# Optimization experiments

Hardware: AMD Instinct MI355X
Metric: run time of the kernel (lower is better)

The kernel has to match this reference:

```python
import jax, jax.numpy as jnp
import numpy as np

B, T, IMG, P, D, H, L = 4, 32, 84, 14, 768, 12, 3
GP = IMG // P            # 6 patches per side
NP = GP * GP             # 36 patches
N = NP + 1               # +cls token
FF = 4 * D
HD = D // H


def _ln(x, g, b):
    m = jnp.mean(x, -1, keepdims=True)
    v = jnp.var(x, -1, keepdims=True)
    return (x - m) * jax.lax.rsqrt(v + 1e-5) * g + b


def _mha(x, qkv_w, qkv_b, proj_w, proj_b):
    Bn, Nn, C = x.shape
    qkv = (x @ qkv_w + qkv_b).reshape(Bn, Nn, 3, H, HD).transpose(2, 0, 3, 1, 4)
    q, k, v = qkv[0], qkv[1], qkv[2]                      # (B,H,N,hd)
    attn = jax.nn.softmax(jnp.einsum('bhqd,bhkd->bhqk', q, k) * HD ** -0.5, axis=-1)
    o = jnp.einsum('bhqk,bhkd->bhqd', attn, v).transpose(0, 2, 1, 3).reshape(Bn, Nn, C)
    return o @ proj_w + proj_b


def _blocks(x, pre_g, pre_b, n1_g, n1_b, qkv_w, qkv_b, proj_w, proj_b,
            n2_g, n2_b, fc1_w, fc1_b, fc2_w, fc2_b):
    # TemporalViT applies an extra pre-norm, then x = x + Block(x_norm),
    # where Block itself contains two residual sublayers on x_norm.
    for i in range(L):
        xn = _ln(x, pre_g[i], pre_b[i])
        y = xn + _mha(_ln(xn, n1_g[i], n1_b[i]), qkv_w[i], qkv_b[i], proj_w[i], proj_b[i])
        h = jax.nn.gelu(_ln(y, n2_g[i], n2_b[i]) @ fc1_w[i] + fc1_b[i], approximate=False)
        y = y + h @ fc2_w[i] + fc2_b[i]
        x = x + y
    return x


def _forward(x, conv_w, conv_b, cls, pos, tpos,
             s_pre_g, s_pre_b, s_n1_g, s_n1_b, s_qkv_w, s_qkv_b, s_proj_w, s_proj_b,
             s_n2_g, s_n2_b, s_fc1_w, s_fc1_b, s_fc2_w, s_fc2_b,
             t_pre_g, t_pre_b, t_n1_g, t_n1_b, t_qkv_w, t_qkv_b, t_proj_w, t_proj_b,
             t_n2_g, t_n2_b, t_fc1_w, t_fc1_b, t_fc2_w, t_fc2_b):
    xf = x.reshape(B * T, 3, IMG, IMG)
    p = jax.lax.conv_general_dilated(xf, conv_w, (P, P), 'VALID',
                                     dimension_numbers=('NCHW', 'OIHW', 'NCHW'))
    p = p + conv_b[None, :, None, None]                  # (BT, D, 6, 6)
    p = p.reshape(B * T, D, NP).transpose(0, 2, 1)       # (BT, 36, D)
    p = jnp.concatenate([jnp.broadcast_to(cls, (B * T, 1, D)), p], axis=1) + pos
    p = _blocks(p, s_pre_g, s_pre_b, s_n1_g, s_n1_b, s_qkv_w, s_qkv_b, s_proj_w,
                s_proj_b, s_n2_g, s_n2_b, s_fc1_w, s_fc1_b, s_fc2_w, s_fc2_b)
    p = p.reshape(B, T * N, D)
    tp = jnp.broadcast_to(tpos[:, :T, None, :], (1, T, N, D)).reshape(1, T * N, D)
    p = p + tp
    p = _blocks(p, t_pre_g, t_pre_b, t_n1_g, t_n1_b, t_qkv_w, t_qkv_b, t_proj_w,
                t_proj_b, t_n2_g, t_n2_b, t_fc1_w, t_fc1_b, t_fc2_w, t_fc2_b)
    return p.mean(axis=1)                                # (B, D)


def setup_inputs() -> dict:
    key = jax.random.key(0)
    ks = iter(jax.random.split(key, 64))
    r = lambda shape, s=0.02: (jax.random.normal(next(ks), shape, jnp.float32) * s)
    inp = {
        'x': jax.random.normal(next(ks), (B, T, 3, IMG, IMG), jnp.float32),
        'conv_w': r((D, 3, P, P)), 'conv_b': jnp.zeros((D,), jnp.float32),
        'cls': r((1, 1, D)), 'pos': r((1, N, D)), 'tpos': r((1, 100, D)),
    }
    for pfx in ('s', 't'):
        inp[f'{pfx}_pre_g'] = jnp.ones((L, D), jnp.float32)
        inp[f'{pfx}_pre_b'] = jnp.zeros((L, D), jnp.float32)
        inp[f'{pfx}_n1_g'] = jnp.ones((L, D), jnp.float32)
        inp[f'{pfx}_n1_b'] = jnp.zeros((L, D), jnp.float32)
        inp[f'{pfx}_qkv_w'] = r((L, D, 3 * D))
        inp[f'{pfx}_qkv_b'] = jnp.zeros((L, 3 * D), jnp.float32)
        inp[f'{pfx}_proj_w'] = r((L, D, D))
        inp[f'{pfx}_proj_b'] = jnp.zeros((L, D), jnp.float32)
        inp[f'{pfx}_n2_g'] = jnp.ones((L, D), jnp.float32)
        inp[f'{pfx}_n2_b'] = jnp.zeros((L, D), jnp.float32)
        inp[f'{pfx}_fc1_w'] = r((L, D, FF))
        inp[f'{pfx}_fc1_b'] = jnp.zeros((L, FF), jnp.float32)
        inp[f'{pfx}_fc2_w'] = r((L, FF, D))
        inp[f'{pfx}_fc2_b'] = jnp.zeros((L, D), jnp.float32)
    return inp


def reference(x, conv_w, conv_b, cls, pos, tpos,
              s_pre_g, s_pre_b, s_n1_g, s_n1_b, s_qkv_w, s_qkv_b, s_proj_w, s_proj_b,
              s_n2_g, s_n2_b, s_fc1_w, s_fc1_b, s_fc2_w, s_fc2_b,
              t_pre_g, t_pre_b, t_n1_g, t_n1_b, t_qkv_w, t_qkv_b, t_proj_w, t_proj_b,
              t_n2_g, t_n2_b, t_fc1_w, t_fc1_b, t_fc2_w, t_fc2_b):
    return _forward(x, conv_w, conv_b, cls, pos, tpos,
                    s_pre_g, s_pre_b, s_n1_g, s_n1_b, s_qkv_w, s_qkv_b, s_proj_w,
                    s_proj_b, s_n2_g, s_n2_b, s_fc1_w, s_fc1_b, s_fc2_w, s_fc2_b,
                    t_pre_g, t_pre_b, t_n1_g, t_n1_b, t_qkv_w, t_qkv_b, t_proj_w,
                    t_proj_b, t_n2_g, t_n2_b, t_fc1_w, t_fc1_b, t_fc2_w, t_fc2_b)
```

## Files before the change

kernel.cpp:

```cpp
#include <hip/hip_runtime.h>
#include <math.h>

#define NTOK 4736
#define DM   768
#define NHEAD 12
#define KC   640

typedef __attribute__((ext_vector_type(8))) short bf16x8;
typedef __attribute__((ext_vector_type(4))) float f32x4;

__device__ inline short f2bf(float f) {
  union { float f; unsigned u; } v; v.f = f;
  unsigned r = v.u + 0x7FFF + ((v.u >> 16) & 1);
  return (short)(r >> 16);
}
__device__ inline float bf2f(short s) {
  union { unsigned u; float f; } v; v.u = ((unsigned)(unsigned short)s) << 16;
  return v.f;
}

__device__ inline void gload16(const void* g, void* l) {
  __builtin_amdgcn_global_load_lds(
      (const __attribute__((address_space(1))) void*)g,
      (__attribute__((address_space(3))) void*)l, 16, 0, 0);
}

__global__ __launch_bounds__(256) void im2col_k(const float* __restrict__ x,
                                                short* __restrict__ col) {
  int i = blockIdx.x * 256 + threadIdx.x;
  int r = i / KC, k = i % KC;
  short v = 0;
  if (k < 588) {
    int bt = r / 36, p = r % 36;
    int gy = p / 6, gx = p % 6;
    int c = k / 196, rem = k % 196;
    int ky = rem / 14, kx = rem % 14;
    v = f2bf(x[(((size_t)bt * 3 + c) * 84 + gy * 14 + ky) * 84 + gx * 14 + kx]);
  }
  col[i] = v;
}

__global__ __launch_bounds__(256) void convw_k(const float* __restrict__ w,
                                               short* __restrict__ out) {
  int i = blockIdx.x * 256 + threadIdx.x;
  int n = i / KC, k = i % KC;
  out[i] = (k < 588) ? f2bf(w[(size_t)n * 588 + k]) : (short)0;
}

__global__ __launch_bounds__(256) void wt_k(const float* __restrict__ in,
                                            short* __restrict__ out,
                                            int K, int N) {
  __shared__ float tile[32][33];
  const int l = blockIdx.z;
  in  += (size_t)l * K * N;
  out += (size_t)l * N * K;
  const int n0 = blockIdx.x * 32, k0 = blockIdx.y * 32;
  const int tx = threadIdx.x & 31, ty = threadIdx.x >> 5;
#pragma unroll
  for (int r = 0; r < 4; r++)
    tile[ty + 8 * r][tx] = in[(size_t)(k0 + ty + 8 * r) * N + n0 + tx];
  __syncthreads();
#pragma unroll
  for (int r = 0; r < 4; r++)
    out[(size_t)(n0 + ty + 8 * r) * K + k0 + tx] = f2bf(tile[tx][ty + 8 * r]);
}

__global__ __launch_bounds__(256) void assemble_k(const float* __restrict__ conv_out,
                                                  const float* __restrict__ cls,
                                                  const float* __restrict__ pos,
                                                  float* __restrict__ X) {
  int i = blockIdx.x * 256 + threadIdx.x;
  int t = i / DM, d = i % DM;
  int bt = t / 37, n = t % 37;
  float v = (n == 0) ? cls[d] : conv_out[((size_t)bt * 36 + (n - 1)) * DM + d];
  X[i] = v + pos[n * DM + d];
}

__global__ __launch_bounds__(256) void tpos_k(float* __restrict__ X,
                                              const float* __restrict__ tpos) {
  int i = blockIdx.x * 256 + threadIdx.x;
  int row = i / DM, d = i % DM;
  int tt = (row % 1184) / 37;
  X[i] += tpos[tt * DM + d];
}

template <bool OBF>
__global__ __launch_bounds__(256) void ln_k(const float* __restrict__ in,
                                            const float* __restrict__ g,
                                            const float* __restrict__ b,
                                            void* __restrict__ outp) {
  int r = blockIdx.x;
  int tid = threadIdx.x;
  const float* xr = in + (size_t)r * DM;
  float v0 = xr[tid], v1 = xr[tid + 256], v2 = xr[tid + 512];
  float s  = v0 + v1 + v2;
  float sq = v0 * v0 + v1 * v1 + v2 * v2;
#pragma unroll
  for (int off = 32; off; off >>= 1) {
    s  += __shfl_down(s, off);
    sq += __shfl_down(sq, off);
  }
  __shared__ float ss[4], sg[4];
  if ((tid & 63) == 0) { ss[tid >> 6] = s; sg[tid >> 6] = sq; }
  __syncthreads();
  float S = ss[0] + ss[1] + ss[2] + ss[3];
  float Q = sg[0] + sg[1] + sg[2] + sg[3];
  float mean = S * (1.f / 768.f);
  float var  = Q * (1.f / 768.f) - mean * mean;
  float rs = rsqrtf(var + 1e-5f);
  float o0 = (v0 - mean) * rs * g[tid]       + b[tid];
  float o1 = (v1 - mean) * rs * g[tid + 256] + b[tid + 256];
  float o2 = (v2 - mean) * rs * g[tid + 512] + b[tid + 512];
  if (OBF) {
    short* o = (short*)outp + (size_t)r * DM;
    o[tid] = f2bf(o0); o[tid + 256] = f2bf(o1); o[tid + 512] = f2bf(o2);
  } else {
    float* o = (float*)outp + (size_t)r * DM;
    o[tid] = o0; o[tid + 256] = o1; o[tid + 512] = o2;
  }
}

__global__ __launch_bounds__(256) void ln2_k(const float* __restrict__ in,
                                             const float* __restrict__ g1,
                                             const float* __restrict__ b1,
                                             const float* __restrict__ g2,
                                             const float* __restrict__ b2,
                                             float* __restrict__ xn,
                                             short* __restrict__ w) {
  int r = blockIdx.x;
  int tid = threadIdx.x;
  const float* xr = in + (size_t)r * DM;
  float v0 = xr[tid], v1 = xr[tid + 256], v2 = xr[tid + 512];
  float s  = v0 + v1 + v2;
  float sq = v0 * v0 + v1 * v1 + v2 * v2;
#pragma unroll
  for (int off = 32; off; off >>= 1) {
    s  += __shfl_down(s, off);
    sq += __shfl_down(sq, off);
  }
  __shared__ float ss[4], sg[4], ss2[4], sg2[4];
  if ((tid & 63) == 0) { ss[tid >> 6] = s; sg[tid >> 6] = sq; }
  __syncthreads();
  float S = ss[0] + ss[1] + ss[2] + ss[3];
  float Q = sg[0] + sg[1] + sg[2] + sg[3];
  float mean = S * (1.f / 768.f);
  float var  = Q * (1.f / 768.f) - mean * mean;
  float rs = rsqrtf(var + 1e-5f);
  float x0 = (v0 - mean) * rs * g1[tid]       + b1[tid];
  float x1 = (v1 - mean) * rs * g1[tid + 256] + b1[tid + 256];
  float x2 = (v2 - mean) * rs * g1[tid + 512] + b1[tid + 512];
  float* xo = xn + (size_t)r * DM;
  xo[tid] = x0; xo[tid + 256] = x1; xo[tid + 512] = x2;
  float s2  = x0 + x1 + x2;
  float sq2 = x0 * x0 + x1 * x1 + x2 * x2;
#pragma unroll
  for (int off = 32; off; off >>= 1) {
    s2  += __shfl_down(s2, off);
    sq2 += __shfl_down(sq2, off);
  }
  if ((tid & 63) == 0) { ss2[tid >> 6] = s2; sg2[tid >> 6] = sq2; }
  __syncthreads();
  float S2 = ss2[0] + ss2[1] + ss2[2] + ss2[3];
  float Q2 = sg2[0] + sg2[1] + sg2[2] + sg2[3];
  float mean2 = S2 * (1.f / 768.f);
  float var2  = Q2 * (1.f / 768.f) - mean2 * mean2;
  float rs2 = rsqrtf(var2 + 1e-5f);
  short* wo = w + (size_t)r * DM;
  wo[tid]       = f2bf((x0 - mean2) * rs2 * g2[tid]       + b2[tid]);
  wo[tid + 256] = f2bf((x1 - mean2) * rs2 * g2[tid + 256] + b2[tid + 256]);
  wo[tid + 512] = f2bf((x2 - mean2) * rs2 * g2[tid + 512] + b2[tid + 512]);
}

template <int BM, int BN, bool GELU, bool OBF, bool HASR1, bool HASR2>
__global__ __launch_bounds__(256, 4) void tgemm_k(const short* __restrict__ A,
                                                  const short* __restrict__ Bw,
                                                  const float* __restrict__ bias,
                                                  const float* __restrict__ r1,
                                                  const float* __restrict__ r2,
                                                  void* __restrict__ Cout,
                                                  int M, int N, int K) {
  constexpr int TM = BM / 2, TN = BN / 2;
  constexpr int MF = TM / 16, NF = TN / 16;
  constexpr int ACH = BM / 64, BCH = BN / 64;
  constexpr int LOADS = ACH + BCH;

  __shared__ short As[2][BM][32];
  __shared__ short Bs[2][BN][32];

  const int nwg  = gridDim.x * gridDim.y;
  const int orig = blockIdx.x + gridDim.x * blockIdx.y;
  const int qq = nwg >> 3, rrm = nwg & 7;
  const int xcd = orig & 7, sub = orig >> 3;
  const int wgid = ((xcd < rrm) ? xcd * (qq + 1) : rrm * (qq + 1) + (xcd - rrm) * qq) + sub;
  const int bm = (wgid / gridDim.y) * BM, bn = (wgid % gridDim.y) * BN;

  const int tid = threadIdx.x, wid = tid >> 6, lane = tid & 63;
  const int lr = lane & 15, lg = lane >> 4;
  const int wm = wid >> 1, wn = wid & 1;

  const int srow = tid >> 2;
  const int sslot = (tid & 3) ^ ((srow >> 1) & 3);
  const short* Asrc = A  + (size_t)(bm + srow) * K + sslot * 8;
  const short* Bsrc = Bw + (size_t)(bn + srow) * K + sslot * 8;

  f32x4 acc[MF][NF];
#pragma unroll
  for (int m = 0; m < MF; m++)
#pragma unroll
    for (int n = 0; n < NF; n++) acc[m][n] = (f32x4){0.f, 0.f, 0.f, 0.f};

#define STAGE(slot, kk)                                                        \
  do {                                                                         \
    _Pragma("unroll")                                                          \
    for (int j = 0; j < ACH; j++)                                              \
      gload16(Asrc + (size_t)(j * 64) * K + (kk),                              \
              (char*)&As[slot][0][0] + j * 4096 + wid * 1024);                 \
    _Pragma("unroll")                                                          \
    for (int j = 0; j < BCH; j++)                                              \
      gload16(Bsrc + (size_t)(j * 64) * K + (kk),                              \
              (char*)&Bs[slot][0][0] + j * 4096 + wid * 1024);                 \
  } while (0)

  const int NT = K >> 5;
  const int rkey = (lr >> 1) & 3;

  STAGE(0, 0);
  for (int t = 0; t < NT; t++) {
    const int c = t & 1;
    if (t + 1 < NT) {
      STAGE(c ^ 1, (t + 1) << 5);
      if constexpr (LOADS == 4) asm volatile("s_waitcnt vmcnt(4)" ::: "memory");
      else                      asm volatile("s_waitcnt vmcnt(2)" ::: "memory");
    } else {
      asm volatile("s_waitcnt vmcnt(0)" ::: "memory");
    }
    __builtin_amdgcn_s_barrier();

    bf16x8 aq[MF], bq[NF];
#pragma unroll
    for (int nf = 0; nf < NF; nf++) {
      const int row = wn * TN + nf * 16 + lr;
      bq[nf] = *reinterpret_cast<const bf16x8*>(
          (const char*)&Bs[c][0][0] + row * 64 + ((lg ^ rkey) << 4));
    }
#pragma unroll
    for (int mf = 0; mf < MF; mf++) {
      const int row = wm * TM + mf * 16 + lr;
      aq[mf] = *reinterpret_cast<const bf16x8*>(
          (const char*)&As[c][0][0] + row * 64 + ((lg ^ rkey) << 4));
    }
    __builtin_amdgcn_s_setprio(1);
#pragma unroll
    for (int mf = 0; mf < MF; mf++)
#pragma unroll
      for (int nf = 0; nf < NF; nf++)
        acc[mf][nf] = __builtin_amdgcn_mfma_f32_16x16x32_bf16(
            aq[mf], bq[nf], acc[mf][nf], 0, 0, 0);
    __builtin_amdgcn_s_setprio(0);
    __builtin_amdgcn_s_barrier();
  }
#undef STAGE

#pragma unroll
  for (int m = 0; m < MF; m++) {
#pragma unroll
    for (int r = 0; r < 4; r++) {
      int row = bm + wm * TM + m * 16 + lg * 4 + r;
      if (row < M) {
#pragma unroll
        for (int n = 0; n < NF; n++) {
          int col = bn + wn * TN + n * 16 + lr;
          size_t idx = (size_t)row * N + col;
          float v = acc[m][n][r];
          if (bias) v += bias[col];
          if (GELU) v = 0.5f * v * (1.f + erff(v * 0.70710678118654752f));
          if (HASR1) v += r1[idx];
          if (HASR2) v += r2[idx];
          if (OBF) ((short*)Cout)[idx] = f2bf(v);
          else     ((float*)Cout)[idx] = v;
        }
      }
    }
  }
}

__global__ __launch_bounds__(256) void attn_k(const short* __restrict__ qkv,
                                              short* __restrict__ out,
                                              int Bn, int Nn) {
  const int gx = gridDim.x, gy = gridDim.y;
  const int nwg = gx * gy;
  const int orig = blockIdx.x + gx * blockIdx.y;
  const int qq = nwg >> 3, rrm = nwg & 7;
  const int xcd = orig & 7, sub = orig >> 3;
  const int wgid = ((xcd < rrm) ? xcd * (qq + 1) : rrm * (qq + 1) + (xcd - rrm) * qq) + sub;
  const int bh = wgid / gy;
  const int qb = wgid % gy;
  const int b = bh / NHEAD, h = bh % NHEAD;
  const int q0 = qb * 64;

  const int tid = threadIdx.x;
  const int wid = tid >> 6, lane = tid & 63;
  const int lr = lane & 15, lg = lane >> 4;

  __shared__ short Ks[128][64];
  __shared__ short Vt[64][128];
  __shared__ short Ps[4][16][128];

  const int qrow_in = q0 + wid * 16 + lr;
  const int qcl = (qrow_in < Nn) ? qrow_in : (Nn - 1);
  const short* qp = qkv + ((size_t)(b * Nn + qcl)) * 2304 + h * 64 + lg * 8;
  bf16x8 qa0 = *reinterpret_cast<const bf16x8*>(qp);
  bf16x8 qa1 = *reinterpret_cast<const bf16x8*>(qp + 32);
#pragma unroll
  for (int j = 0; j < 8; j++) {
    qa0[j] = f2bf(bf2f(qa0[j]) * 0.125f);
    qa1[j] = f2bf(bf2f(qa1[j]) * 0.125f);
  }

  f32x4 oo[4];
#pragma unroll
  for (int dg = 0; dg < 4; dg++) oo[dg] = (f32x4){0.f, 0.f, 0.f, 0.f};
  float mm[4] = {-1e30f, -1e30f, -1e30f, -1e30f};
  float ll[4] = {0.f, 0.f, 0.f, 0.f};

  const int skey = tid >> 1;
  const int sdq  = (tid & 1) * 32;
  const int vkeyc = tid & 127;
  const int vd0   = (tid >> 7) * 32;
  const int swr = (lr & 7) << 3;
  const int ksw = (skey & 7) << 3;

  for (int k0 = 0; k0 < Nn; k0 += 128) {
    {
      int kg = k0 + skey; if (kg >= Nn) kg = Nn - 1;
      const short* kp = qkv + ((size_t)(b * Nn + kg)) * 2304 + 768 + h * 64 + sdq;
      bf16x8 k0v = *reinterpret_cast<const bf16x8*>(kp);
      bf16x8 k1v = *reinterpret_cast<const bf16x8*>(kp + 8);
      bf16x8 k2v = *reinterpret_cast<const bf16x8*>(kp + 16);
      bf16x8 k3v = *reinterpret_cast<const bf16x8*>(kp + 24);
      *reinterpret_cast<bf16x8*>(&Ks[skey][(sdq +  0) ^ ksw]) = k0v;
      *reinterpret_cast<bf16x8*>(&Ks[skey][(sdq +  8) ^ ksw]) = k1v;
      *reinterpret_cast<bf16x8*>(&Ks[skey][(sdq + 16) ^ ksw]) = k2v;
      *reinterpret_cast<bf16x8*>(&Ks[skey][(sdq + 24) ^ ksw]) = k3v;
      int vg = k0 + vkeyc; if (vg >= Nn) vg = Nn - 1;
      const short* vp = qkv + ((size_t)(b * Nn + vg)) * 2304 + 1536 + h * 64 + vd0;
      bf16x8 v0 = *reinterpret_cast<const bf16x8*>(vp);
      bf16x8 v1 = *reinterpret_cast<const bf16x8*>(vp + 8);
      bf16x8 v2 = *reinterpret_cast<const bf16x8*>(vp + 16);
      bf16x8 v3 = *reinterpret_cast<const bf16x8*>(vp + 24);
#pragma unroll
      for (int i = 0; i < 8; i++) {
        Vt[vd0 + i]     [vkeyc ^ (i << 3)] = v0[i];
        Vt[vd0 + 8 + i] [vkeyc ^ (i << 3)] = v1[i];
        Vt[vd0 + 16 + i][vkeyc ^ (i << 3)] = v2[i];
        Vt[vd0 + 24 + i][vkeyc ^ (i << 3)] = v3[i];
      }
    }
    __syncthreads();

    f32x4 c[8];
#pragma unroll
    for (int kf = 0; kf < 8; kf++) {
      c[kf] = (f32x4){0.f, 0.f, 0.f, 0.f};
      const short* krow = &Ks[kf * 16 + lr][0];
      bf16x8 kq0 = *reinterpret_cast<const bf16x8*>(krow + ((lg * 8) ^ swr));
      c[kf] = __builtin_amdgcn_mfma_f32_16x16x32_bf16(qa0, kq0, c[kf], 0, 0, 0);
      bf16x8 kq1 = *reinterpret_cast<const bf16x8*>(krow + ((32 + lg * 8) ^ swr));
      c[kf] = __builtin_amdgcn_mfma_f32_16x16x32_bf16(qa1, kq1, c[kf], 0, 0, 0);
    }
#pragma unroll
    for (int kf = 0; kf < 8; kf++) {
      if (k0 + kf * 16 + lr >= Nn)
        c[kf][0] = c[kf][1] = c[kf][2] = c[kf][3] = -1e30f;
    }

    float tr[4];
#pragma unroll
    for (int r = 0; r < 4; r++) {
      float tv = fmaxf(fmaxf(fmaxf(c[0][r], c[1][r]), fmaxf(c[2][r], c[3][r])),
                       fmaxf(fmaxf(c[4][r], c[5][r]), fmaxf(c[6][r], c[7][r])));
      tv = fmaxf(tv, __shfl_xor(tv, 1, 16));
      tv = fmaxf(tv, __shfl_xor(tv, 2, 16));
      tv = fmaxf(tv, __shfl_xor(tv, 4, 16));
      tv = fmaxf(tv, __shfl_xor(tv, 8, 16));
      tr[r] = tv;
    }
    const bool skipall = __all((tr[0] - mm[0] <= 8.f) & (tr[1] - mm[1] <= 8.f) &
                               (tr[2] - mm[2] <= 8.f) & (tr[3] - mm[3] <= 8.f));
#pragma unroll
    for (int r = 0; r < 4; r++) {
      if (!skipall) {
        float mn = fmaxf(mm[r], tr[r]);
        float sc = __expf(mm[r] - mn);
        ll[r] *= sc;
        oo[0][r] *= sc; oo[1][r] *= sc; oo[2][r] *= sc; oo[3][r] *= sc;
        mm[r] = mn;
      }
      float p[8], ps = 0.f;
#pragma unroll
      for (int kf = 0; kf < 8; kf++) {
        p[kf] = __expf(c[kf][r] - mm[r]);
        ps += p[kf];
      }
      ps += __shfl_xor(ps, 1, 16);
      ps += __shfl_xor(ps, 2, 16);
      ps += __shfl_xor(ps, 4, 16);
      ps += __shfl_xor(ps, 8, 16);
      ll[r] += ps;
      const int prow = lg * 4 + r;
      const int psw  = (prow & 7) << 3;
      short* pr = &Ps[wid][prow][0];
#pragma unroll
      for (int kf = 0; kf < 8; kf++)
        pr[(kf * 16 + lr) ^ psw] = f2bf(p[kf]);
    }

#pragma unroll
    for (int ks = 0; ks < 4; ks++) {
      bf16x8 pa = *reinterpret_cast<const bf16x8*>(
          &Ps[wid][lr][(ks * 32 + lg * 8) ^ swr]);
#pragma unroll
      for (int dg = 0; dg < 4; dg++) {
        bf16x8 vq = *reinterpret_cast<const bf16x8*>(
            &Vt[dg * 16 + lr][(ks * 32 + lg * 8) ^ swr]);
        oo[dg] = __builtin_amdgcn_mfma_f32_16x16x32_bf16(pa, vq, oo[dg], 0, 0, 0);
      }
    }
    __syncthreads();
  }

#pragma unroll
  for (int r = 0; r < 4; r++) {
    int qr = q0 + wid * 16 + lg * 4 + r;
    if (qr < Nn) {
      float inv = 1.f / ll[r];
      short* op = out + ((size_t)(b * Nn + qr)) * DM + h * 64 + lr;
      op[0]  = f2bf(oo[0][r] * inv);
      op[16] = f2bf(oo[1][r] * inv);
      op[32] = f2bf(oo[2][r] * inv);
      op[48] = f2bf(oo[3][r] * inv);
    }
  }
}

__global__ __launch_bounds__(256) void mean1_k(const float* __restrict__ X,
                                               float* __restrict__ P) {
  int b = blockIdx.x, seg = blockIdx.z;
  int d = blockIdx.y * 256 + threadIdx.x;
  int r0 = seg * 148;
  float s = 0.f;
  for (int r = r0; r < r0 + 148; r++) s += X[((size_t)b * 1184 + r) * DM + d];
  P[((size_t)(b * 8 + seg)) * DM + d] = s;
}
__global__ __launch_bounds__(256) void mean2_k(const float* __restrict__ P,
                                               float* __restrict__ out) {
  int b = blockIdx.x;
  int d = blockIdx.y * 256 + threadIdx.x;
  float s = 0.f;
#pragma unroll
  for (int seg = 0; seg < 8; seg++) s += P[((size_t)(b * 8 + seg)) * DM + d];
  out[b * DM + d] = s * (1.f / 1184.f);
}

extern "C" void kernel_launch(void* const* d_in, const int* in_sizes, int n_in,
                              void* d_out, int out_size, void* d_ws, size_t ws_size,
                              hipStream_t stream) {
  (void)in_sizes; (void)n_in; (void)out_size; (void)ws_size;
  const float* x      = (const float*)d_in[0];
  const float* conv_w = (const float*)d_in[1];
  const float* conv_b = (const float*)d_in[2];
  const float* cls    = (const float*)d_in[3];
  const float* pos    = (const float*)d_in[4];
  const float* tpos   = (const float*)d_in[5];
  const float* W[2][14];
  for (int p = 0; p < 2; p++)
    for (int i = 0; i < 14; i++)
      W[p][i] = (const float*)d_in[6 + p * 14 + i];

  char* ws = (char*)d_ws;
  const size_t TOKF = (size_t)NTOK * DM * 4;
  float* X    = (float*)(ws);
  float* XN   = (float*)(ws + TOKF);
  float* Y    = (float*)(ws + 2 * TOKF);
  short* TA2  = (short*)(ws + 3 * TOKF);
  short* BIG  = (short*)(ws + 3 * TOKF + (size_t)NTOK * DM * 2);
  short* WB   = (short*)(ws + 3 * TOKF + (size_t)NTOK * DM * 2
                            + (size_t)NTOK * 3072 * 2);
  const size_t QE = (size_t)3 * 2304 * 768;
  const size_t PE = (size_t)3 * 768 * 768;
  const size_t F1E = (size_t)3 * 3072 * 768;
  const size_t F2E = (size_t)3 * 768 * 3072;
  const size_t PFX = QE + PE + F1E + F2E;
  short* WQ[2], *WP[2], *WF1[2], *WF2[2];
  for (int p = 0; p < 2; p++) {
    WQ[p]  = WB + p * PFX;
    WP[p]  = WQ[p] + QE;
    WF1[p] = WP[p] + PE;
    WF2[p] = WF1[p] + F1E;
  }
  short* CW = WB + 2 * PFX;
  float* PB = (float*)(CW + (size_t)768 * KC);

  for (int p = 0; p < 2; p++) {
    wt_k<<<dim3(72, 24, 3), 256, 0, stream>>>(W[p][4],  WQ[p],  768, 2304);
    wt_k<<<dim3(24, 24, 3), 256, 0, stream>>>(W[p][6],  WP[p],  768, 768);
    wt_k<<<dim3(96, 24, 3), 256, 0, stream>>>(W[p][10], WF1[p], 768, 3072);
    wt_k<<<dim3(24, 96, 3), 256, 0, stream>>>(W[p][12], WF2[p], 3072, 768);
  }
  convw_k<<<1920, 256, 0, stream>>>(conv_w, CW);

  im2col_k<<<11520, 256, 0, stream>>>(x, BIG);
  tgemm_k<64, 64, false, false, false, false><<<dim3(72, 12), 256, 0, stream>>>(
      BIG, CW, conv_b, nullptr, nullptr, Y, 4608, 768, KC);
  assemble_k<<<14208, 256, 0, stream>>>(Y, cls, pos, X);

  for (int phase = 0; phase < 2; phase++) {
    const int Bn = (phase == 0) ? 128 : 4;
    const int Nn = (phase == 0) ? 37 : 1184;
    if (phase == 1) tpos_k<<<14208, 256, 0, stream>>>(X, tpos);
    for (int i = 0; i < 3; i++) {
      const float* pre_g = W[phase][0] + i * DM;
      const float* pre_b = W[phase][1] + i * DM;
      const float* n1_g  = W[phase][2] + i * DM;
      const float* n1_b  = W[phase][3] + i * DM;
      const float* qkv_b = W[phase][5] + i * 2304;
      const float* prj_b = W[phase][7] + i * DM;
      const float* n2_g  = W[phase][8] + i * DM;
      const float* n2_b  = W[phase][9] + i * DM;
      const float* fc1_b = W[phase][11] + i * 3072;
      const float* fc2_b = W[phase][13] + i * DM;
      const short* qkv_w = WQ[phase]  + (size_t)i * 2304 * 768;
      const short* prj_w = WP[phase]  + (size_t)i * 768 * 768;
      const short* fc1_w = WF1[phase] + (size_t)i * 3072 * 768;
      const short* fc2_w = WF2[phase] + (size_t)i * 768 * 3072;

      ln2_k<<<NTOK, 256, 0, stream>>>(X, pre_g, pre_b, n1_g, n1_b, XN, TA2);
      tgemm_k<128, 128, false, true, false, false><<<dim3(37, 18), 256, 0, stream>>>(
          TA2, qkv_w, qkv_b, nullptr, nullptr, BIG, NTOK, 2304, DM);
      attn_k<<<dim3(Bn * NHEAD, (Nn + 63) / 64), 256, 0, stream>>>(BIG, TA2, Bn, Nn);
      tgemm_k<64, 64, false, false, true, false><<<dim3(74, 12), 256, 0, stream>>>(
          TA2, prj_w, prj_b, XN, nullptr, Y, NTOK, DM, DM);
      ln_k<true><<<NTOK, 256, 0, stream>>>(Y, n2_g, n2_b, TA2);
      tgemm_k<128, 128, true, true, false, false><<<dim3(37, 24), 256, 0, stream>>>(
          TA2, fc1_w, fc1_b, nullptr, nullptr, BIG, NTOK, 3072, DM);
      tgemm_k<64, 64, false, false, true, true><<<dim3(74, 12), 256, 0, stream>>>(
          BIG, fc2_w, fc2_b, Y, X, X, NTOK, DM, 3072);
    }
  }
  mean1_k<<<dim3(4, 3, 8), 256, 0, stream>>>(X, PB);
  mean2_k<<<dim3(4, 3), 256, 0, stream>>>(PB, (float*)d_out);
}
```

Baseline: 1.505 ms.

## Triple-buffer GEMM k-loop and add 64-key attention kernel for spatial phase

The GEMM main loop moves from a two-slot to a three-slot LDS ring, prefetching two k-tiles ahead with adjusted vmcnt waits to hide more global-load latency. The extra LDS slot raises per-block shared memory, which may lower occupancy under the 4-block launch bound. Separately, a new attention kernel with 64-key tiles is used for the spatial phase (37 tokens), so it no longer stages and computes over 128-key tiles that are mostly padding. The original 128-key kernel is kept for the temporal phase.

```diff
diff --git a/kernel.cpp b/kernel.cpp
--- a/kernel.cpp
+++ b/kernel.cpp
@@ -184,8 +184,8 @@
   constexpr int ACH = BM / 64, BCH = BN / 64;
   constexpr int LOADS = ACH + BCH;
 
-  __shared__ short As[2][BM][32];
-  __shared__ short Bs[2][BN][32];
+  __shared__ short As[3][BM][32];
+  __shared__ short Bs[3][BN][32];
 
   const int nwg  = gridDim.x * gridDim.y;
   const int orig = blockIdx.x + gridDim.x * blockIdx.y;
@@ -225,12 +225,16 @@
   const int rkey = (lr >> 1) & 3;
 
   STAGE(0, 0);
+  STAGE(1, 32);
+  int c = 0, sst = 2;
   for (int t = 0; t < NT; t++) {
-    const int c = t & 1;
-    if (t + 1 < NT) {
-      STAGE(c ^ 1, (t + 1) << 5);
-      if constexpr (LOADS == 4) asm volatile("s_waitcnt vmcnt(4)" ::: "memory");
-      else                      asm volatile("s_waitcnt vmcnt(2)" ::: "memory");
+    if (t + 2 < NT) {
+      STAGE(sst, (t + 2) << 5);
+      if constexpr (LOADS == 2) asm volatile("s_waitcnt vmcnt(4)" ::: "memory");
+      else                      asm volatile("s_waitcnt vmcnt(8)" ::: "memory");
+    } else if (t + 1 < NT) {
+      if constexpr (LOADS == 2) asm volatile("s_waitcnt vmcnt(2)" ::: "memory");
+      else                      asm volatile("s_waitcnt vmcnt(4)" ::: "memory");
     } else {
       asm volatile("s_waitcnt vmcnt(0)" ::: "memory");
     }
@@ -258,6 +262,8 @@
             aq[mf], bq[nf], acc[mf][nf], 0, 0, 0);
     __builtin_amdgcn_s_setprio(0);
     __builtin_amdgcn_s_barrier();
+    c   = (c   == 2) ? 0 : c + 1;
+    sst = (sst == 2) ? 0 : sst + 1;
   }
 #undef STAGE
 
@@ -284,9 +290,156 @@
   }
 }
 
-__global__ __launch_bounds__(256) void attn_k(const short* __restrict__ qkv,
-                                              short* __restrict__ out,
-                                              int Bn, int Nn) {
+__global__ __launch_bounds__(256) void attn64_k(const short* __restrict__ qkv,
+                                                short* __restrict__ out,
+                                                int Bn, int Nn) {
+  const int gx = gridDim.x, gy = gridDim.y;
+  const int nwg = gx * gy;
+  const int orig = blockIdx.x + gx * blockIdx.y;
+  const int qq = nwg >> 3, rrm = nwg & 7;
+  const int xcd = orig & 7, sub = orig >> 3;
+  const int wgid = ((xcd < rrm) ? xcd * (qq + 1) : rrm * (qq + 1) + (xcd - rrm) * qq) + sub;
+  const int bh = wgid / gy;
+  const int qb = wgid % gy;
+  const int b = bh / NHEAD, h = bh % NHEAD;
+  const int q0 = qb * 64;
+
+  const int tid = threadIdx.x;
+  const int wid = tid >> 6, lane = tid & 63;
+  const int lr = lane & 15, lg = lane >> 4;
+
+  __shared__ short Ks[64][64];
+  __shared__ short Vt[64][64];
+  __shared__ short Ps[4][16][64];
+
+  const int qrow_in = q0 + wid * 16 + lr;
+  const int qcl = (qrow_in < Nn) ? qrow_in : (Nn - 1);
+  const short* qp = qkv + ((size_t)(b * Nn + qcl)) * 2304 + h * 64 + lg * 8;
+  bf16x8 qa0 = *reinterpret_cast<const bf16x8*>(qp);
+  bf16x8 qa1 = *reinterpret_cast<const bf16x8*>(qp + 32);
+
+  f32x4 oo[4];
+#pragma unroll
+  for (int dg = 0; dg < 4; dg++) oo[dg] = (f32x4){0.f, 0.f, 0.f, 0.f};
+  float mm[4] = {-1e30f, -1e30f, -1e30f, -1e30f};
+  float ll[4] = {0.f, 0.f, 0.f, 0.f};
+
+  const int skey = tid >> 2;
+  const int sdq  = (tid & 3) * 16;
+  const int vkey = tid & 63;
+  const int vd0  = wid * 16;
+
+  const int swr = (lr & 7) << 3;
+
+  for (int k0 = 0; k0 < Nn; k0 += 64) {
+    {
+      int kg = k0 + skey; if (kg >= Nn) kg = Nn - 1;
+      const short* kp = qkv + ((size_t)(b * Nn + kg)) * 2304 + 768 + h * 64 + sdq;
+      bf16x8 ka = *reinterpret_cast<const bf16x8*>(kp);
+      bf16x8 kb = *reinterpret_cast<const bf16x8*>(kp + 8);
+      const int ksw = (skey & 7) << 3;
+      *reinterpret_cast<bf16x8*>(&Ks[skey][sdq ^ ksw])       = ka;
+      *reinterpret_cast<bf16x8*>(&Ks[skey][(sdq + 8) ^ ksw]) = kb;
+      int vg = k0 + vkey; if (vg >= Nn) vg = Nn - 1;
+      const short* vp = qkv + ((size_t)(b * Nn + vg)) * 2304 + 1536 + h * 64 + vd0;
+      bf16x8 va = *reinterpret_cast<const bf16x8*>(vp);
+      bf16x8 vb = *reinterpret_cast<const bf16x8*>(vp + 8);
+#pragma unroll
+      for (int i = 0; i < 8; i++) {
+        Vt[vd0 + i][vkey ^ (i << 3)]     = va[i];
+        Vt[vd0 + 8 + i][vkey ^ (i << 3)] = vb[i];
+      }
+    }
+    __syncthreads();
+
+    f32x4 c[4];
+#pragma unroll
+    for (int kf = 0; kf < 4; kf++) {
+      c[kf] = (f32x4){0.f, 0.f, 0.f, 0.f};
+      const short* krow = &Ks[kf * 16 + lr][0];
+      bf16x8 kb0 = *reinterpret_cast<const bf16x8*>(krow + ((lg * 8) ^ swr));
+      c[kf] = __builtin_amdgcn_mfma_f32_16x16x32_bf16(qa0, kb0, c[kf], 0, 0, 0);
+      bf16x8 kb1 = *reinterpret_cast<const bf16x8*>(krow + ((32 + lg * 8) ^ swr));
+      c[kf] = __builtin_amdgcn_mfma_f32_16x16x32_bf16(qa1, kb1, c[kf], 0, 0, 0);
+    }
+#pragma unroll
+    for (int kf = 0; kf < 4; kf++) {
+#pragma unroll
+      for (int r = 0; r < 4; r++) c[kf][r] *= 0.125f;
+      if (k0 + kf * 16 + lr >= Nn)
+        c[kf][0] = c[kf][1] = c[kf][2] = c[kf][3] = -1e30f;
+    }
+
+    float tr[4];
+#pragma unroll
+    for (int r = 0; r < 4; r++) {
+      float tv = fmaxf(fmaxf(c[0][r], c[1][r]), fmaxf(c[2][r], c[3][r]));
+      tv = fmaxf(tv, __shfl_xor(tv, 1, 16));
+      tv = fmaxf(tv, __shfl_xor(tv, 2, 16));
+      tv = fmaxf(tv, __shfl_xor(tv, 4, 16));
+      tv = fmaxf(tv, __shfl_xor(tv, 8, 16));
+      tr[r] = tv;
+    }
+    const bool skipall = __all((tr[0] - mm[0] <= 8.f) & (tr[1] - mm[1] <= 8.f) &
+                               (tr[2] - mm[2] <= 8.f) & (tr[3] - mm[3] <= 8.f));
+#pragma unroll
+    for (int r = 0; r < 4; r++) {
+      if (!skipall) {
+        float mn = fmaxf(mm[r], tr[r]);
+        float sc = __expf(mm[r] - mn);
+        ll[r] *= sc;
+        oo[0][r] *= sc; oo[1][r] *= sc; oo[2][r] *= sc; oo[3][r] *= sc;
+        mm[r] = mn;
+      }
+      float p0 = __expf(c[0][r] - mm[r]);
+      float p1 = __expf(c[1][r] - mm[r]);
+      float p2 = __expf(c[2][r] - mm[r]);
+      float p3 = __expf(c[3][r] - mm[r]);
+      float ps = (p0 + p1) + (p2 + p3);
+      ps += __shfl_xor(ps, 1, 16);
+      ps += __shfl_xor(ps, 2, 16);
+      ps += __shfl_xor(ps, 4, 16);
+      ps += __shfl_xor(ps, 8, 16);
+      ll[r] += ps;
+      const int prow = lg * 4 + r;
+      const int psw  = (prow & 7) << 3;
+      short* pr = &Ps[wid][prow][0];
+      pr[lr ^ psw]        = f2bf(p0);
+      pr[(16 + lr) ^ psw] = f2bf(p1);
+      pr[(32 + lr) ^ psw] = f2bf(p2);
+      pr[(48 + lr) ^ psw] = f2bf(p3);
+    }
+
+#pragma unroll
+    for (int ks = 0; ks < 2; ks++) {
+      bf16x8 pa = *reinterpret_cast<const bf16x8*>(&Ps[wid][lr][(ks * 32 + lg * 8) ^ swr]);
+#pragma unroll
+      for (int dg = 0; dg < 4; dg++) {
+        bf16x8 vb = *reinterpret_cast<const bf16x8*>(
+            &Vt[dg * 16 + lr][(ks * 32 + lg * 8) ^ swr]);
+        oo[dg] = __builtin_amdgcn_mfma_f32_16x16x32_bf16(pa, vb, oo[dg], 0, 0, 0);
+      }
+    }
+    __syncthreads();
+  }
+
+#pragma unroll
+  for (int r = 0; r < 4; r++) {
+    int qr = q0 + wid * 16 + lg * 4 + r;
+    if (qr < Nn) {
+      float inv = 1.f / ll[r];
+      short* op = out + ((size_t)(b * Nn + qr)) * DM + h * 64 + lr;
+      op[0]  = f2bf(oo[0][r] * inv);
+      op[16] = f2bf(oo[1][r] * inv);
+      op[32] = f2bf(oo[2][r] * inv);
+      op[48] = f2bf(oo[3][r] * inv);
+    }
+  }
+}
+
+__global__ __launch_bounds__(256) void attn128_k(const short* __restrict__ qkv,
+                                                 short* __restrict__ out,
+                                                 int Bn, int Nn) {
   const int gx = gridDim.x, gy = gridDim.y;
   const int nwg = gx * gy;
   const int orig = blockIdx.x + gx * blockIdx.y;
@@ -537,7 +690,10 @@
       ln2_k<<<NTOK, 256, 0, stream>>>(X, pre_g, pre_b, n1_g, n1_b, XN, TA2);
       tgemm_k<128, 128, false, true, false, false><<<dim3(37, 18), 256, 0, stream>>>(
           TA2, qkv_w, qkv_b, nullptr, nullptr, BIG, NTOK, 2304, DM);
-      attn_k<<<dim3(Bn * NHEAD, (Nn + 63) / 64), 256, 0, stream>>>(BIG, TA2, Bn, Nn);
+      if (phase == 0)
+        attn64_k<<<dim3(Bn * NHEAD, (Nn + 63) / 64), 256, 0, stream>>>(BIG, TA2, Bn, Nn);
+      else
+        attn128_k<<<dim3(Bn * NHEAD, (Nn + 63) / 64), 256, 0, stream>>>(BIG, TA2, Bn, Nn);
       tgemm_k<64, 64, false, false, true, false><<<dim3(74, 12), 256, 0, stream>>>(
           TA2, prj_w, prj_b, XN, nullptr, Y, NTOK, DM, DM);
       ln_k<true><<<NTOK, 256, 0, stream>>>(Y, n2_g, n2_b, TA2);
```

New measurement: 1.616 ms. +7.4%, slower.
